# Optimization experiments

Hardware: AMD Instinct MI355X
Metric: run time of the kernel (lower is better)

## Reference

```python
import jax, jax.numpy as jnp
import numpy as np

B, N, D = 2, 8192, 1024
H, DH = 8, 64  # heads, dim_head; inner = H*DH = 512
INNER = H * DH


def setup_inputs() -> dict:
    key = jax.random.key(0)
    k1, k2, k3 = jax.random.split(key, 3)
    x = jax.random.normal(k1, (B, N, D), dtype=jnp.float32)
    # xavier_uniform-ish scaling for weights
    W_qkv = jax.random.normal(k2, (D, 3 * INNER), dtype=jnp.float32) * (1.0 / np.sqrt(D))
    W_out = jax.random.normal(k3, (INNER, D), dtype=jnp.float32) * (1.0 / np.sqrt(INNER))
    b_out = jnp.zeros((D,), dtype=jnp.float32)
    return {"x": x, "W_qkv": W_qkv, "W_out": W_out, "b_out": b_out}


def reference(x, W_qkv, W_out, b_out):
    b, n, d = x.shape
    qkv = x @ W_qkv                               # [b, n, 3*inner]
    q, k, v = jnp.split(qkv, 3, axis=-1)          # each [b, n, inner]

    def to_heads(t):
        return t.reshape(b, n, H, DH).transpose(0, 2, 1, 3)  # [b, h, n, dh]

    q, k, v = to_heads(q), to_heads(k), to_heads(v)
    q = jax.nn.softmax(q, axis=-1)                # over dim_head
    k = jax.nn.softmax(k, axis=-2)                # over sequence
    # context: k^T v  -> [b, h, dh, dh]
    context = jnp.einsum('bhnd,bhne->bhde', k, v)
    out = jnp.einsum('bhnd,bhde->bhne', q, context)  # [b, h, n, dh]
    out = out.transpose(0, 2, 1, 3).reshape(b, n, INNER)
    return out @ W_out + b_out                    # [b, n, d]
```

## Files before the change

kernel.cpp:

```cpp
#include <hip/hip_runtime.h>
#include <stdint.h>


typedef _Float16 half4 __attribute__((ext_vector_type(4)));
typedef _Float16 half8 __attribute__((ext_vector_type(8)));
typedef float f32x4 __attribute__((ext_vector_type(4)));

#define WS_XB 0UL
#define WS_WQKVT 33554432UL
#define WS_CWT 37748736UL
#define WS_CTXPART 54525952UL
#define WS_COLPART 71303168UL
#define WS_SQ 88080384UL

__device__ __forceinline__ void gld16(const void* g, void* l) {
  __builtin_amdgcn_global_load_lds(
      (const __attribute__((address_space(1))) unsigned int*)g,
      (__attribute__((address_space(3))) unsigned int*)l, 16, 0, 0);
}

__global__ void prep_kernel(const float* __restrict__ x,
                            const float* __restrict__ Wqkv,
                            _Float16* __restrict__ xb,
                            _Float16* __restrict__ wqkvT) {
  const int blk = blockIdx.x;
  if (blk < 16384) {
    int i = blk * 256 + threadIdx.x;
    f32x4 v = *(const f32x4*)(x + (size_t)i * 4);
    half4 h = {(_Float16)v[0], (_Float16)v[1], (_Float16)v[2], (_Float16)v[3]};
    *(half4*)(xb + (size_t)i * 4) = h;
  } else {
    int i = (blk - 16384) * 256 + threadIdx.x;
    int c = i >> 10, r = i & 1023;
    wqkvT[i] = (_Float16)Wqkv[(size_t)r * 1536 + c];
  }
}


__device__ __forceinline__ void stage_tile(const _Float16* __restrict__ G, int K,
                                           int rowbase, int kt, char* region,
                                           int t) {
  char* wbase = region + (t & ~63) * 16;
#pragma unroll
  for (int q = 0; q < 4; ++q) {
    const int row = q * 32 + (t >> 3);
    const int col8 = ((t & 7) ^ (row & 7)) * 8;
    gld16(G + (size_t)(rowbase + row) * K + kt + col8, wbase + q * 4096);
  }
}

__device__ __forceinline__ void stage_tile64(const _Float16* __restrict__ G,
                                             int K, int rowbase, int kt,
                                             char* region, int t) {
  char* wbase = region + (t & ~63) * 16;
#pragma unroll
  for (int q = 0; q < 2; ++q) {
    const int row = q * 32 + (t >> 3);
    const int col8 = ((t & 7) ^ (row & 7)) * 8;
    gld16(G + (size_t)(rowbase + row) * K + kt + col8, wbase + q * 4096);
  }
}

template <int EPI>
__global__ __launch_bounds__(256, 2) void gemm128(
    const _Float16* __restrict__ A, const _Float16* __restrict__ BT, int K,
    int NTN, int bstride, _Float16* __restrict__ oQ,
    float* __restrict__ ctxpart, float* __restrict__ colpart,
    float* __restrict__ oC, const float* __restrict__ bias) {
  __shared__ char lds[65536];
  const int t = threadIdx.x;
  const int l = t & 63, w = t >> 6;
  const int wm = w >> 1, wn = w & 1;
  const int fr = l & 15, qq = l >> 4;
  const int swzx = (fr & 7) << 4;

  const int nwg = gridDim.x;
  const int cpx = nwg >> 3;
  const int wg = (blockIdx.x & 7) * cpx + (blockIdx.x >> 3);
  const int tileM = wg / NTN, tileN = wg - tileM * NTN;
  const int mbase = tileM * 128, nbase = tileN * 128;
  BT += (size_t)(tileM >> 6) * bstride;

  const int NT = K >> 6;
  f32x4 acc[4][4] = {};
  half8 a[4][2], b[4][2];

  auto STG = [&](int tile) {
    int kt = tile * 64;
    if (kt > K - 64) kt = K - 64;
    char* base = lds + ((tile & 1) << 15);
    stage_tile(A, K, mbase, kt, base, t);
    if (EPI == 1 || tileN < 4) {
      stage_tile(BT, K, nbase, kt, base + 16384, t);
    } else {
      const int h = tileN - 4;
      stage_tile64(BT, K, 512 + h * 64, kt, base + 16384, t);
      stage_tile64(BT, K, 1024 + h * 64, kt, base + 16384 + 8192, t);
    }
  };

  STG(0);
  STG(1);
  asm volatile("s_waitcnt vmcnt(8)" ::: "memory");
  __builtin_amdgcn_s_barrier();

  for (int t2 = 0; t2 < NT; ++t2) {
    const char* ldsA = lds + ((t2 & 1) << 15);
    const char* ldsB = ldsA + 16384;
    STG(t2 + 1);
#pragma unroll
    for (int mi = 0; mi < 4; ++mi)
#pragma unroll
      for (int kk = 0; kk < 2; ++kk) {
        int off = (wm * 64 + mi * 16 + fr) * 128 + ((kk * 64 + qq * 16) ^ swzx);
        a[mi][kk] = *(const half8*)(ldsA + off);
      }
#pragma unroll
    for (int ni = 0; ni < 4; ++ni)
#pragma unroll
      for (int kk = 0; kk < 2; ++kk) {
        int off = (wn * 64 + ni * 16 + fr) * 128 + ((kk * 64 + qq * 16) ^ swzx);
        b[ni][kk] = *(const half8*)(ldsB + off);
      }
    __builtin_amdgcn_s_barrier();
    __builtin_amdgcn_s_setprio(1);
#pragma unroll
    for (int mi = 0; mi < 4; ++mi)
#pragma unroll
      for (int ni = 0; ni < 2; ++ni)
#pragma unroll
        for (int kk = 0; kk < 2; ++kk)
          acc[mi][ni] = __builtin_amdgcn_mfma_f32_16x16x32_f16(
              a[mi][kk], b[ni][kk], acc[mi][ni], 0, 0, 0);
    __builtin_amdgcn_s_setprio(0);
    asm volatile("s_waitcnt vmcnt(0) lgkmcnt(0)" ::: "memory");
    __builtin_amdgcn_s_barrier();
    __builtin_amdgcn_s_setprio(1);
#pragma unroll
    for (int mi = 0; mi < 4; ++mi)
#pragma unroll
      for (int ni = 2; ni < 4; ++ni)
#pragma unroll
        for (int kk = 0; kk < 2; ++kk)
          acc[mi][ni] = __builtin_amdgcn_mfma_f32_16x16x32_f16(
              a[mi][kk], b[ni][kk], acc[mi][ni], 0, 0, 0);
    __builtin_amdgcn_s_setprio(0);
  }

  if (EPI == 0) {
    if (tileN < 4) {
      const int gcol0 = nbase + wn * 64;
#pragma unroll
      for (int mi = 0; mi < 4; ++mi) {
        const int grow = mbase + wm * 64 + mi * 16 + qq * 4;
        float e[4][4], rs[4];
#pragma unroll
        for (int r = 0; r < 4; ++r) {
          float s = 0.f;
#pragma unroll
          for (int ni = 0; ni < 4; ++ni) {
            e[ni][r] = __expf(acc[mi][ni][r]);
            s += e[ni][r];
          }
#pragma unroll
          for (int off = 1; off < 16; off <<= 1) s += __shfl_xor(s, off, 64);
          rs[r] = 1.f / s;
        }
#pragma unroll
        for (int ni = 0; ni < 4; ++ni) {
          const int gcol = gcol0 + ni * 16 + fr;
#pragma unroll
          for (int r = 0; r < 4; ++r)
            oQ[(size_t)(grow + r) * 512 + gcol] = (_Float16)(e[ni][r] * rs[r]);
        }
      }
    } else {
      const int h = tileN - 4;
      float* sf = (float*)lds;
#pragma unroll
      for (int mi = 0; mi < 4; ++mi) {
        const int n = wm * 64 + mi * 16 + qq * 4;
#pragma unroll
        for (int ni = 0; ni < 4; ++ni) {
          const int c = wn * 64 + ni * 16 + fr;
#pragma unroll
          for (int r = 0; r < 4; ++r) {
            float v = acc[mi][ni][r];
            if (wn == 0) v = __expf(v);
            sf[(size_t)(n + r) * 128 + c] = v;
          }
        }
      }
      __syncthreads();
      const int d0 = (t & 15) * 4, e0 = (t >> 4) * 4;
      f32x4 cacc = {0.f, 0.f, 0.f, 0.f};
      float pacc[4][4] = {};
      for (int n = 0; n < 128; ++n) {
        f32x4 ek4 = *(const f32x4*)&sf[(size_t)n * 128 + d0];
        f32x4 vv4 = *(const f32x4*)&sf[(size_t)n * 128 + 64 + e0];
        cacc += ek4;
#pragma unroll
        for (int i = 0; i < 4; ++i)
#pragma unroll
          for (int j = 0; j < 4; ++j) pacc[i][j] += ek4[i] * vv4[j];
      }
      const int bh = (tileM >> 6) * 8 + h, chunk = tileM & 63;
      float* cp = ctxpart + ((size_t)bh * 64 + chunk) * 4096;
#pragma unroll
      for (int i = 0; i < 4; ++i) {
        f32x4 o = {pacc[i][0], pacc[i][1], pacc[i][2], pacc[i][3]};
        *(f32x4*)&cp[(d0 + i) * 64 + e0] = o;
      }
      if (t < 16)
        *(f32x4*)&colpart[((size_t)bh * 64 + chunk) * 64 + d0] = cacc;
    }
  } else {
#pragma unroll
    for (int mi = 0; mi < 4; ++mi) {
      const int grow = mbase + wm * 64 + mi * 16 + qq * 4;
#pragma unroll
      for (int ni = 0; ni < 4; ++ni) {
        const int gcol = nbase + wn * 64 + ni * 16 + fr;
        const float bb = bias[gcol];
#pragma unroll
        for (int r = 0; r < 4; ++r)
          oC[(size_t)(grow + r) * 1024 + gcol] = acc[mi][ni][r] + bb;
      }
    }
  }
}

__global__ __launch_bounds__(256) void ctxw_kernel(
    const float* __restrict__ ctxpart, const float* __restrict__ colpart,
    const float* __restrict__ Wout, _Float16* __restrict__ cwT) {
  __shared__ float part[4][64];
  __shared__ float csp[64];
  __shared__ float crow[64];
  const int blk = blockIdx.x;
  const int bh = blk >> 6, d = blk & 63;
  const int b = bh >> 3, h = bh & 7;
  const int t = threadIdx.x;
  const int e = t & 63, cq = t >> 6;
  float p = 0.f;
#pragma unroll
  for (int cc = 0; cc < 16; ++cc)
    p += ctxpart[((size_t)bh * 64 + cq * 16 + cc) * 4096 + d * 64 + e];
  part[cq][e] = p;
  if (t >= 64 && t < 128)
    csp[t - 64] = colpart[((size_t)bh * 64 + (t - 64)) * 64 + d];
  __syncthreads();
  if (t < 64) {
    float csum = 0.f;
#pragma unroll
    for (int c = 0; c < 64; ++c) csum += csp[c];
    crow[t] = (part[0][t] + part[1][t] + part[2][t] + part[3][t]) / csum;
  }
  __syncthreads();
  float acc[4] = {};
  for (int e2 = 0; e2 < 64; ++e2) {
    const float c = crow[e2];
    const float* wr = Wout + (size_t)(h * 64 + e2) * 1024 + t;
#pragma unroll
    for (int j = 0; j < 4; ++j) acc[j] += c * wr[j * 256];
  }
  _Float16* dst = cwT + (size_t)b * 524288 + (size_t)t * 512 + h * 64 + d;
#pragma unroll
  for (int j = 0; j < 4; ++j) dst[(size_t)j * 256 * 512] = (_Float16)acc[j];
}

extern "C" void kernel_launch(void* const* d_in, const int* in_sizes, int n_in,
                              void* d_out, int out_size, void* d_ws, size_t ws_size,
                              hipStream_t stream) {
  const float* x = (const float*)d_in[0];
  const float* Wqkv = (const float*)d_in[1];
  const float* Wout = (const float*)d_in[2];
  const float* bout = (const float*)d_in[3];
  float* out = (float*)d_out;
  char* ws = (char*)d_ws;

  _Float16* xb = (_Float16*)(ws + WS_XB);
  _Float16* wqkvT = (_Float16*)(ws + WS_WQKVT);
  _Float16* cwT = (_Float16*)(ws + WS_CWT);
  _Float16* sq = (_Float16*)(ws + WS_SQ);
  float* ctxpart = (float*)(ws + WS_CTXPART);
  float* colpart = (float*)(ws + WS_COLPART);

  prep_kernel<<<22528, 256, 0, stream>>>(x, Wqkv, xb, wqkvT);
  gemm128<0><<<1536, 256, 0, stream>>>(xb, wqkvT, 1024, 12, 0, sq, ctxpart,
                                       colpart, nullptr, nullptr);
  ctxw_kernel<<<1024, 256, 0, stream>>>(ctxpart, colpart, Wout, cwT);
  gemm128<1><<<1024, 256, 0, stream>>>(sq, cwT, 512, 8, 524288, nullptr,
                                       nullptr, nullptr, out, bout);
}
```

Before: 151.7 us.

## Compute per-chunk K^T V context with fp16 MFMA instead of scalar FMA loop

The per-tile context reduction (exp(K)^T V over 128 rows) used to stage fp32 values in LDS and run a 128-iteration scalar outer-product loop per thread. It now packs exp(K) and V into swizzled fp16 LDS tiles and computes the 64x64 context with 16x16x32 f16 MFMA instructions. Column sums are reduced in registers with shuffles plus a small LDS buffer. This lowers precision of the context partials to fp16 inputs, and exp values could lose accuracy or overflow in fp16.

```diff
diff --git a/kernel.cpp b/kernel.cpp
--- a/kernel.cpp
+++ b/kernel.cpp
@@ -176,43 +176,77 @@
       }
     } else {
       const int h = tileN - 4;
-      float* sf = (float*)lds;
+      float* credu = (float*)(lds + 32768);
+      if (wn == 0) {
+#pragma unroll
+        for (int mi = 0; mi < 4; ++mi)
+#pragma unroll
+          for (int ni = 0; ni < 4; ++ni) {
+            f32x4 e4;
+#pragma unroll
+            for (int r = 0; r < 4; ++r) e4[r] = __expf(acc[mi][ni][r]);
+            acc[mi][ni] = e4;
+          }
+        float s[4] = {};
+#pragma unroll
+        for (int ni = 0; ni < 4; ++ni) {
+#pragma unroll
+          for (int mi = 0; mi < 4; ++mi)
+#pragma unroll
+            for (int r = 0; r < 4; ++r) s[ni] += acc[mi][ni][r];
+          s[ni] += __shfl_xor(s[ni], 16, 64);
+          s[ni] += __shfl_xor(s[ni], 32, 64);
+        }
+        if (l < 16) {
+#pragma unroll
+          for (int ni = 0; ni < 4; ++ni) credu[wm * 64 + ni * 16 + fr] = s[ni];
+        }
+      }
+      {
+        char* dst8 = lds + (wn ? 16384 : 0);
+#pragma unroll
+        for (int mi = 0; mi < 4; ++mi) {
+          const int nb = (wm * 64 + mi * 16 + qq * 4) * 2;
+#pragma unroll
+          for (int ni = 0; ni < 4; ++ni) {
+            const int c = ni * 16 + fr;
+            half4 pk = {(_Float16)acc[mi][ni][0], (_Float16)acc[mi][ni][1],
+                        (_Float16)acc[mi][ni][2], (_Float16)acc[mi][ni][3]};
+            *(half4*)(dst8 + c * 256 + (nb ^ ((c & 15) << 4))) = pk;
+          }
+        }
+      }
+      __syncthreads();
+      half8 bf[4];
+      const int erow = w * 16 + fr;
+#pragma unroll
+      for (int kk = 0; kk < 4; ++kk)
+        bf[kk] = *(const half8*)(lds + 16384 + erow * 256 +
+                                 ((kk * 64 + qq * 16) ^ ((erow & 15) << 4)));
+      f32x4 dacc[4] = {};
 #pragma unroll
       for (int mi = 0; mi < 4; ++mi) {
-        const int n = wm * 64 + mi * 16 + qq * 4;
-#pragma unroll
-        for (int ni = 0; ni < 4; ++ni) {
-          const int c = wn * 64 + ni * 16 + fr;
-#pragma unroll
-          for (int r = 0; r < 4; ++r) {
-            float v = acc[mi][ni][r];
-            if (wn == 0) v = __expf(v);
-            sf[(size_t)(n + r) * 128 + c] = v;
-          }
-        }
-      }
-      __syncthreads();
-      const int d0 = (t & 15) * 4, e0 = (t >> 4) * 4;
-      f32x4 cacc = {0.f, 0.f, 0.f, 0.f};
-      float pacc[4][4] = {};
-      for (int n = 0; n < 128; ++n) {
-        f32x4 ek4 = *(const f32x4*)&sf[(size_t)n * 128 + d0];
-        f32x4 vv4 = *(const f32x4*)&sf[(size_t)n * 128 + 64 + e0];
-        cacc += ek4;
-#pragma unroll
-        for (int i = 0; i < 4; ++i)
-#pragma unroll
-          for (int j = 0; j < 4; ++j) pacc[i][j] += ek4[i] * vv4[j];
+        const int drow = mi * 16 + fr;
+#pragma unroll
+        for (int kk = 0; kk < 4; ++kk) {
+          half8 af = *(const half8*)(lds + drow * 256 +
+                                     ((kk * 64 + qq * 16) ^ ((drow & 15) << 4)));
+          dacc[mi] =
+              __builtin_amdgcn_mfma_f32_16x16x32_f16(af, bf[kk], dacc[mi], 0, 0, 0);
+        }
       }
       const int bh = (tileM >> 6) * 8 + h, chunk = tileM & 63;
       float* cp = ctxpart + ((size_t)bh * 64 + chunk) * 4096;
 #pragma unroll
-      for (int i = 0; i < 4; ++i) {
-        f32x4 o = {pacc[i][0], pacc[i][1], pacc[i][2], pacc[i][3]};
-        *(f32x4*)&cp[(d0 + i) * 64 + e0] = o;
-      }
-      if (t < 16)
-        *(f32x4*)&colpart[((size_t)bh * 64 + chunk) * 64 + d0] = cacc;
+      for (int mi = 0; mi < 4; ++mi)
+#pragma unroll
+        for (int r = 0; r < 4; ++r)
+          cp[(mi * 16 + qq * 4 + r) * 64 + w * 16 + fr] = dacc[mi][r];
+      if (t < 16) {
+        f32x4 c0 = *(const f32x4*)&credu[t * 4];
+        f32x4 c1 = *(const f32x4*)&credu[64 + t * 4];
+        *(f32x4*)&colpart[((size_t)bh * 64 + chunk) * 64 + t * 4] = c0 + c1;
+      }
     }
   } else {
 #pragma unroll
```

Result: faster. 135.9 us (-10.4%).
